# Optimization experiments

Hardware: AMD Instinct MI355X
Metric: run time of the kernel (lower is better)

Reference implementation:

```python
import jax, jax.numpy as jnp
import numpy as np

NUM_EXPERTS = 8
TOP_K = 2

def setup_inputs() -> dict:
    key = jax.random.key(0)
    ks = jax.random.split(key, 5)
    B, S, H, I, E = 4, 2048, 1024, 2816, NUM_EXPERTS
    return {
        "hidden_states": jax.random.normal(ks[0], (B, S, H), dtype=jnp.float32),
        "gate_w": jax.random.normal(ks[1], (H, E), dtype=jnp.float32) / np.sqrt(H),
        "w_gate": jax.random.normal(ks[2], (E, H, I), dtype=jnp.float32) / np.sqrt(H),
        "w_up": jax.random.normal(ks[3], (E, H, I), dtype=jnp.float32) / np.sqrt(H),
        "w_down": jax.random.normal(ks[4], (E, I, H), dtype=jnp.float32) / np.sqrt(I),
    }

def reference(hidden_states, gate_w, w_gate, w_up, w_down):
    B, S, H = hidden_states.shape
    x = hidden_states.reshape(-1, H)                      # [T, H]
    router_logits = x @ gate_w                            # [T, E]
    probs = jax.nn.softmax(router_logits.astype(jnp.float32), axis=-1)
    topk_w, sel = jax.lax.top_k(probs, TOP_K)             # [T, K]
    topk_w = topk_w / jnp.sum(topk_w, axis=-1, keepdims=True)
    topk_w = topk_w.astype(x.dtype)
    out = jnp.zeros_like(x)
    for e in range(NUM_EXPERTS):
        # combine weight for this expert per token (0 if not routed)
        we = jnp.sum(jnp.where(sel == e, topk_w, 0.0), axis=-1)  # [T]
        h = jax.nn.silu(x @ w_gate[e]) * (x @ w_up[e])           # [T, I]
        out = out + (h @ w_down[e]) * we[:, None]
    return out.reshape(B, S, H), router_logits
```

## Files before the change

### kernel.cpp

```cpp
#include <hip/hip_runtime.h>
#include <hip/hip_bf16.h>
#include <stdint.h>

typedef unsigned short u16;
typedef unsigned int u32;

#define T_TOK 8192
#define H_DIM 1024
#define I_DIM 2816
#define NE 8

typedef __bf16 bf16x8 __attribute__((ext_vector_type(8)));
typedef float f32x4 __attribute__((ext_vector_type(4)));

union F8 { uint4 v; bf16x8 f; u32 w[4]; };

__device__ __forceinline__ u16 f2bf(float f) {
    u32 u = __float_as_uint(f);
    u32 r = u + 0x7FFFu + ((u >> 16) & 1u);
    return (u16)(r >> 16);
}
__device__ __forceinline__ u32 pkbf(float a, float b) {
    float2 f; f.x = a; f.y = b;
    __hip_bfloat162 h = __float22bfloat162_rn(f);
    union { __hip_bfloat162 h2; u32 w; } cv; cv.h2 = h;
    return cv.w;
}

__device__ __forceinline__ void g2l16(const void* g, void* l) {
    __builtin_amdgcn_global_load_lds(
        (const __attribute__((address_space(1))) u32*)g,
        (__attribute__((address_space(3))) u32*)l, 16, 0, 0);
}

__global__ void zero_cnt_kernel(int* __restrict__ cnt) {
    if (threadIdx.x < NE) cnt[threadIdx.x] = 0;
}

__global__ void __launch_bounds__(256) zero_out_kernel(float* __restrict__ out0) {
    int gid = blockIdx.x * 256 + threadIdx.x;
    f32x4 z = {0.f, 0.f, 0.f, 0.f};
    ((f32x4*)out0)[gid] = z;
}

__global__ void __launch_bounds__(256) xcvt_kernel(const float* __restrict__ x, u16* __restrict__ xb) {
    size_t gid = (size_t)blockIdx.x * 256 + threadIdx.x;
    const float4* s = (const float4*)x + gid * 2;
    float4 a = s[0], b = s[1];
    uint4 o;
    o.x = pkbf(a.x, a.y); o.y = pkbf(a.z, a.w);
    o.z = pkbf(b.x, b.y); o.w = pkbf(b.z, b.w);
    ((uint4*)xb)[gid] = o;
}

__global__ void __launch_bounds__(256)
pack_kernel(const float* __restrict__ src, u32* __restrict__ dst, int K, int N) {
    int e = blockIdx.z;
    int n0 = blockIdx.x * 64;
    int r0 = blockIdx.y * 128;
    __shared__ float sT[128][65];
    int tid = threadIdx.x;
    const float* sp = src + ((size_t)e * K + r0) * N + n0;
#pragma unroll
    for (int rep = 0; rep < 8; rep++) {
        int row = rep * 16 + (tid >> 4);
        int n4 = (tid & 15) * 4;
        float4 v = *(const float4*)(sp + (size_t)row * N + n4);
        sT[row][n4] = v.x; sT[row][n4 + 1] = v.y; sT[row][n4 + 2] = v.z; sT[row][n4 + 3] = v.w;
    }
    __syncthreads();
    int n = tid >> 2, q = tid & 3;
    u32* dp = dst + ((size_t)e * N + n0 + n) * (size_t)(K >> 1) + (r0 >> 1) + q * 16;
    uint4 o[4];
    u32* ow = (u32*)o;
#pragma unroll
    for (int j = 0; j < 16; j++) {
        int k2 = q * 16 + j;
        ow[j] = pkbf(sT[2 * k2][n], sT[2 * k2 + 1][n]);
    }
#pragma unroll
    for (int j = 0; j < 4; j++) ((uint4*)dp)[j] = o[j];
}

__global__ void __launch_bounds__(256)
router_kernel(const float* __restrict__ x, const float* __restrict__ gw,
              float* __restrict__ logits_out, float* __restrict__ wbuf,
              int* __restrict__ cnt, int* __restrict__ idxlist) {
    int lane = threadIdx.x & 63;
    int t = blockIdx.x * 4 + (threadIdx.x >> 6);
    const float* xr = x + (size_t)t * H_DIM;
    float acc[NE];
#pragma unroll
    for (int e = 0; e < NE; e++) acc[e] = 0.f;
#pragma unroll
    for (int i = 0; i < 16; i++) {
        int hh = i * 64 + lane;
        float xv = xr[hh];
        const float4* grow = (const float4*)(gw + (size_t)hh * NE);
        float4 g0 = grow[0], g1 = grow[1];
        acc[0] += xv * g0.x; acc[1] += xv * g0.y;
        acc[2] += xv * g0.z; acc[3] += xv * g0.w;
        acc[4] += xv * g1.x; acc[5] += xv * g1.y;
        acc[6] += xv * g1.z; acc[7] += xv * g1.w;
    }
#pragma unroll
    for (int m = 32; m >= 1; m >>= 1) {
#pragma unroll
        for (int e = 0; e < NE; e++) acc[e] += __shfl_xor(acc[e], m, 64);
    }
    if (lane == 0) {
        float mx = acc[0];
#pragma unroll
        for (int e = 1; e < NE; e++) mx = fmaxf(mx, acc[e]);
        float p[NE];
#pragma unroll
        for (int e = 0; e < NE; e++) p[e] = __expf(acc[e] - mx);
        float4 l0, l1;
        l0.x = acc[0]; l0.y = acc[1]; l0.z = acc[2]; l0.w = acc[3];
        l1.x = acc[4]; l1.y = acc[5]; l1.z = acc[6]; l1.w = acc[7];
        float4* lrow_p = (float4*)(logits_out + (size_t)t * NE);
        lrow_p[0] = l0; lrow_p[1] = l1;
        int a = 0; float pa = p[0];
#pragma unroll
        for (int e = 1; e < NE; e++) if (p[e] > pa) { a = e; pa = p[e]; }
        int b = -1; float pb = -1.f;
#pragma unroll
        for (int e = 0; e < NE; e++) if (e != a && p[e] > pb) { b = e; pb = p[e]; }
        if (b < 0) { b = a ^ 1; pb = p[b]; }
        float inv = 1.f / (pa + pb);
        wbuf[2 * t]     = pa * inv;
        wbuf[2 * t + 1] = pb * inv;
        int pos = atomicAdd(&cnt[a], 1); idxlist[a * T_TOK + pos] = 2 * t;
        pos = atomicAdd(&cnt[b], 1);     idxlist[b * T_TOK + pos] = 2 * t + 1;
    }
}

__global__ void __launch_bounds__(256, 2)
gateup_kernel(const u16* __restrict__ xb, const u32* __restrict__ wgp,
              const u32* __restrict__ wup, const int* __restrict__ cnt,
              const int* __restrict__ idxlist, u16* __restrict__ hchunk,
              int nbase, int nlen) {
    int NN = nlen >> 7;
    int pid = blockIdx.x;
    int xcd = pid & 7;
    int j = pid >> 3;
    int m = j & 63;
    int gs = j >> 6;
    int g = xcd + (gs << 3);
    int e = g / NN;
    int nb = g - e * NN;
    int c = cnt[e];
    int m0 = m * 128;
    if (m0 >= c) return;
    int n0l = nb * 128;
    int n0g = nbase + n0l;

    __shared__ alignas(16) u16 sA[2][128 * 64];
    __shared__ alignas(16) u32 sB[2][128 * 32];
    int tid = threadIdx.x;
    int wv = tid >> 6;

    int arow = tid >> 3;
    int csw = tid & 7;
    const u16* aP[4];
#pragma unroll
    for (int p = 0; p < 4; p++) {
        int jj = m0 + p * 32 + arow; if (jj > c - 1) jj = c - 1;
        int slot = idxlist[e * T_TOK + jj];
        aP[p] = xb + (size_t)(slot >> 1) * H_DIM + ((csw ^ (arow & 7)) << 3);
    }
    size_t bn = (size_t)e * I_DIM + n0g + arow;
    int bsw = (csw ^ (arow & 7)) << 2;
    const u32* bgB = wgp + bn * 512 + bsw;
    const u32* buB = wup + bn * 512 + bsw;

    auto stage = [&](int k0, int buf, const u32* bB) {
#pragma unroll
        for (int p = 0; p < 4; p++)
            g2l16(aP[p] + k0, &sA[buf][(p * 256 + wv * 64) * 8]);
#pragma unroll
        for (int p = 0; p < 4; p++)
            g2l16(bB + (size_t)p * 32 * 512 + (k0 >> 1), &sB[buf][(p * 256 + wv * 64) * 4]);
    };

    int lane = tid & 63;
    int wm = (tid >> 7) & 1, wn = (tid >> 6) & 1;
    int lrow = lane & 15, quad = lane >> 4;
    f32x4 zero = {0.f, 0.f, 0.f, 0.f};
    f32x4 accg[4][4], accu[4][4];
#pragma unroll
    for (int mi = 0; mi < 4; mi++)
#pragma unroll
        for (int ni = 0; ni < 4; ni++) { accg[mi][ni] = zero; accu[mi][ni] = zero; }

    auto run_pass = [&](const u32* bBc, const u32* bBn, f32x4 (&acc)[4][4]) {
#pragma unroll 2
        for (int k0 = 0; k0 < H_DIM; k0 += 64) {
            int buf = (k0 >> 6) & 1;
            __syncthreads();
            if (k0 + 64 < H_DIM) stage(k0 + 64, buf ^ 1, bBc);
            else if (bBn)        stage(0, buf ^ 1, bBn);
#pragma unroll
            for (int kk = 0; kk < 2; kk++) {
                int cb = kk * 4 + quad;
                bf16x8 af[4]; F8 bf[4];
#pragma unroll
                for (int i = 0; i < 4; i++) {
                    int ra = wm * 64 + i * 16 + lrow;
                    af[i] = *(const bf16x8*)&sA[buf][(size_t)(ra * 8 + (cb ^ (ra & 7))) * 8];
                    int n = wn * 64 + i * 16 + lrow;
                    bf[i].v = *(const uint4*)&sB[buf][(size_t)(n * 8 + (cb ^ (n & 7))) * 4];
                }
#pragma unroll
                for (int mi = 0; mi < 4; mi++)
#pragma unroll
                    for (int ni = 0; ni < 4; ni++)
                        acc[mi][ni] = __builtin_amdgcn_mfma_f32_16x16x32_bf16(af[mi], bf[ni].f, acc[mi][ni], 0, 0, 0);
            }
        }
    };

    stage(0, 0, bgB);
    run_pass(bgB, buB, accg);
    run_pass(buB, nullptr, accu);

    u16* hT = &sA[0][0];
    __syncthreads();
#pragma unroll
    for (int mi = 0; mi < 4; mi++) {
#pragma unroll
        for (int r = 0; r < 4; r++) {
            int row = wm * 64 + mi * 16 + quad * 4 + r;
            int swz = (row & 7) << 3;
#pragma unroll
            for (int ni = 0; ni < 4; ni++) {
                int col = wn * 64 + ni * 16 + lrow;
                float gv = accg[mi][ni][r], uv = accu[mi][ni][r];
                float hv = gv * uv / (1.f + __expf(-gv));
                hT[row * 128 + (col ^ swz)] = f2bf(hv);
            }
        }
    }
    __syncthreads();
    {
        int row = tid & 127, half = tid >> 7;
        int grow = m0 + row;
        if (grow < c) {
            int slot = idxlist[e * T_TOK + grow];
            u16* dst = hchunk + (size_t)slot * nlen + n0l + half * 64;
            int swz = (row & 7) << 3;
#pragma unroll
            for (int j2 = 0; j2 < 8; j2++) {
                int colb = half * 64 + j2 * 8;
                *(uint4*)(dst + j2 * 8) = *(const uint4*)&hT[row * 128 + (colb ^ swz)];
            }
        }
    }
}

__global__ void __launch_bounds__(256, 2)
down_kernel(const u16* __restrict__ hchunk, const u32* __restrict__ wdp,
            const int* __restrict__ cnt, const int* __restrict__ idxlist,
            const float* __restrict__ wbuf, float* __restrict__ out0,
            float* __restrict__ ybuf, int kbase, int klen, int beta) {
    int pid = blockIdx.x;
    int xcd = pid & 7;
    int j = pid >> 3;
    int m = j & 63;
    int gs = j >> 6;
    int g = xcd + (gs << 3);
    int e = g >> 3;
    int nb = g & 7;
    int c = cnt[e];
    int m0 = m * 128;
    if (m0 >= c) return;
    int n0 = nb * 128;

    __shared__ alignas(16) u16 sA[2][128 * 64];
    __shared__ alignas(16) u32 sB[2][128 * 32];
    int tid = threadIdx.x;
    int wv = tid >> 6;

    int arow = tid >> 3;
    int csw = tid & 7;
    const u16* aP[4];
#pragma unroll
    for (int p = 0; p < 4; p++) {
        int jj = m0 + p * 32 + arow; if (jj > c - 1) jj = c - 1;
        int slot = idxlist[e * T_TOK + jj];
        aP[p] = hchunk + (size_t)slot * klen + ((csw ^ (arow & 7)) << 3);
    }
    int bsw = (csw ^ (arow & 7)) << 2;
    const u32* bB = wdp + ((size_t)e * H_DIM + n0 + arow) * 1408 + (kbase >> 1) + bsw;

    auto stage = [&](int k0, int buf) {
#pragma unroll
        for (int p = 0; p < 4; p++)
            g2l16(aP[p] + k0, &sA[buf][(p * 256 + wv * 64) * 8]);
#pragma unroll
        for (int p = 0; p < 4; p++)
            g2l16(bB + (size_t)p * 32 * 1408 + (k0 >> 1), &sB[buf][(p * 256 + wv * 64) * 4]);
    };

    int lane = tid & 63;
    int wm = (tid >> 7) & 1, wn = (tid >> 6) & 1;
    int lrow = lane & 15, quad = lane >> 4;
    f32x4 zero = {0.f, 0.f, 0.f, 0.f};
    f32x4 acc[4][4];
#pragma unroll
    for (int mi = 0; mi < 4; mi++)
#pragma unroll
        for (int ni = 0; ni < 4; ni++) acc[mi][ni] = zero;

    stage(0, 0);
#pragma unroll 2
    for (int k0 = 0; k0 < klen; k0 += 64) {
        int buf = (k0 >> 6) & 1;
        __syncthreads();
        if (k0 + 64 < klen) stage(k0 + 64, buf ^ 1);
#pragma unroll
        for (int kk = 0; kk < 2; kk++) {
            int cb = kk * 4 + quad;
            bf16x8 af[4]; F8 bf[4];
#pragma unroll
            for (int i = 0; i < 4; i++) {
                int ra = wm * 64 + i * 16 + lrow;
                af[i] = *(const bf16x8*)&sA[buf][(size_t)(ra * 8 + (cb ^ (ra & 7))) * 8];
                int n = wn * 64 + i * 16 + lrow;
                bf[i].v = *(const uint4*)&sB[buf][(size_t)(n * 8 + (cb ^ (n & 7))) * 4];
            }
#pragma unroll
            for (int mi = 0; mi < 4; mi++)
#pragma unroll
                for (int ni = 0; ni < 4; ni++)
                    acc[mi][ni] = __builtin_amdgcn_mfma_f32_16x16x32_bf16(af[mi], bf[ni].f, acc[mi][ni], 0, 0, 0);
        }
    }
#pragma unroll
    for (int mi = 0; mi < 4; mi++) {
#pragma unroll
        for (int r = 0; r < 4; r++) {
            int grow = m0 + wm * 64 + mi * 16 + quad * 4 + r;
            if (grow < c) {
                int slot = idxlist[e * T_TOK + grow];
                if (ybuf) {
                    float* yrow = ybuf + (size_t)slot * H_DIM + n0 + wn * 64 + lrow;
                    if (beta) {
#pragma unroll
                        for (int ni = 0; ni < 4; ni++) yrow[ni * 16] += acc[mi][ni][r];
                    } else {
#pragma unroll
                        for (int ni = 0; ni < 4; ni++) yrow[ni * 16] = acc[mi][ni][r];
                    }
                } else {
                    float w = wbuf[slot];
                    float* yrow = out0 + (size_t)(slot >> 1) * H_DIM + n0 + wn * 64 + lrow;
#pragma unroll
                    for (int ni = 0; ni < 4; ni++)
                        atomicAdd(&yrow[ni * 16], w * acc[mi][ni][r]);
                }
            }
        }
    }
}

__global__ void __launch_bounds__(256)
combine_kernel(const float* __restrict__ ybuf, const float* __restrict__ wbuf,
               float* __restrict__ out0) {
    int gid = blockIdx.x * 256 + threadIdx.x;
    int t = gid >> 8;
    int h4 = gid & 255;
    float w0 = wbuf[2 * t], w1 = wbuf[2 * t + 1];
    f32x4 a = ((const f32x4*)(ybuf + (size_t)(2 * t) * H_DIM))[h4];
    f32x4 b = ((const f32x4*)(ybuf + (size_t)(2 * t + 1) * H_DIM))[h4];
    f32x4 o;
#pragma unroll
    for (int i = 0; i < 4; i++) o[i] = w0 * a[i] + w1 * b[i];
    ((f32x4*)(out0 + (size_t)t * H_DIM))[h4] = o;
}

extern "C" void kernel_launch(void* const* d_in, const int* in_sizes, int n_in,
                              void* d_out, int out_size, void* d_ws, size_t ws_size,
                              hipStream_t stream) {
    (void)in_sizes; (void)n_in; (void)out_size;
    const float* x  = (const float*)d_in[0];
    const float* gw = (const float*)d_in[1];
    const float* wg = (const float*)d_in[2];
    const float* wu = (const float*)d_in[3];
    const float* wd = (const float*)d_in[4];
    float* out = (float*)d_out;
    float* logits = out + (size_t)T_TOK * H_DIM;
    char* ws = (char*)d_ws;

    size_t off = 0;
    auto take = [&](size_t sz) { char* p = ws + off; off += (sz + 255) & ~(size_t)255; return p; };
    int* cnt      = (int*)take(NE * 4);
    int* idxlist  = (int*)take((size_t)NE * T_TOK * 4);
    float* wbuf   = (float*)take((size_t)2 * T_TOK * 4);
    u16* xb       = (u16*)take((size_t)T_TOK * H_DIM * 2);
    u32* wgp      = (u32*)take((size_t)NE * I_DIM * 512 * 4);
    u32* wup      = (u32*)take((size_t)NE * I_DIM * 512 * 4);
    u32* wdp      = (u32*)take((size_t)NE * H_DIM * 1408 * 4);
    float* ybuf = nullptr;
    size_t ybytes = (size_t)2 * T_TOK * H_DIM * 4;
    size_t minh   = (size_t)2 * T_TOK * 128 * 2 + 256;
    if (ws_size >= off + ybytes + minh) ybuf = (float*)take(ybytes);
    int ich = I_DIM;
    while (ich > 128 && off + (size_t)2 * T_TOK * ich * 2 > ws_size) ich -= 128;
    u16* hchunk = (u16*)(ws + off);

    zero_cnt_kernel<<<1, 64, 0, stream>>>(cnt);
    if (!ybuf) zero_out_kernel<<<T_TOK * H_DIM / 4 / 256, 256, 0, stream>>>(out);
    pack_kernel<<<dim3(I_DIM / 64, H_DIM / 128, NE), 256, 0, stream>>>(wg, wgp, H_DIM, I_DIM);
    pack_kernel<<<dim3(I_DIM / 64, H_DIM / 128, NE), 256, 0, stream>>>(wu, wup, H_DIM, I_DIM);
    pack_kernel<<<dim3(H_DIM / 64, I_DIM / 128, NE), 256, 0, stream>>>(wd, wdp, I_DIM, H_DIM);
    xcvt_kernel<<<T_TOK * H_DIM / 8 / 256, 256, 0, stream>>>(x, xb);
    router_kernel<<<T_TOK / 4, 256, 0, stream>>>(x, gw, logits, wbuf, cnt, idxlist);
    for (int base = 0; base < I_DIM; base += ich) {
        int len = I_DIM - base; if (len > ich) len = ich;
        int NN = len / 128;
        gateup_kernel<<<64 * NN * NE, 256, 0, stream>>>(xb, wgp, wup, cnt, idxlist, hchunk, base, len);
        down_kernel<<<64 * 8 * NE, 256, 0, stream>>>(hchunk, wdp, cnt, idxlist, wbuf, out, ybuf, base, len, base > 0 ? 1 : 0);
    }
    if (ybuf) combine_kernel<<<T_TOK * H_DIM / 4 / 256, 256, 0, stream>>>(ybuf, wbuf, out);
}
```

Baseline: 1.011 ms.

## Use 256-row tiles with 512 threads and fuse gate/up GEMM passes

Both expert GEMM kernels move from 128x128 tiles on 256 threads to 256x128 tiles on 512 threads (8 waves), and the grid mapping is reduced to match. The gate/up kernel now stages gate and up weight tiles together and accumulates both in one K loop, sharing each A-tile load, instead of running two sequential passes over K. The aim is to cut redundant activation loads and raise data reuse per block. In exchange, shared memory per block roughly doubles, and launch_bounds(512,2) with 128 accumulator registers per thread in gateup may cause register spills or lower occupancy.

```diff
diff --git a/kernel.cpp b/kernel.cpp
--- a/kernel.cpp
+++ b/kernel.cpp
@@ -135,7 +135,7 @@
     }
 }
 
-__global__ void __launch_bounds__(256, 2)
+__global__ void __launch_bounds__(512, 2)
 gateup_kernel(const u16* __restrict__ xb, const u32* __restrict__ wgp,
               const u32* __restrict__ wup, const int* __restrict__ cnt,
               const int* __restrict__ idxlist, u16* __restrict__ hchunk,
@@ -144,19 +144,20 @@
     int pid = blockIdx.x;
     int xcd = pid & 7;
     int j = pid >> 3;
-    int m = j & 63;
-    int gs = j >> 6;
+    int m = j & 31;
+    int gs = j >> 5;
     int g = xcd + (gs << 3);
     int e = g / NN;
     int nb = g - e * NN;
     int c = cnt[e];
-    int m0 = m * 128;
+    int m0 = m * 256;
     if (m0 >= c) return;
     int n0l = nb * 128;
     int n0g = nbase + n0l;
 
-    __shared__ alignas(16) u16 sA[2][128 * 64];
-    __shared__ alignas(16) u32 sB[2][128 * 32];
+    __shared__ alignas(16) u16 sA[2][256 * 64];
+    __shared__ alignas(16) u32 sBg[2][128 * 32];
+    __shared__ alignas(16) u32 sBu[2][128 * 32];
     int tid = threadIdx.x;
     int wv = tid >> 6;
 
@@ -165,7 +166,7 @@
     const u16* aP[4];
 #pragma unroll
     for (int p = 0; p < 4; p++) {
-        int jj = m0 + p * 32 + arow; if (jj > c - 1) jj = c - 1;
+        int jj = m0 + p * 64 + arow; if (jj > c - 1) jj = c - 1;
         int slot = idxlist[e * T_TOK + jj];
         aP[p] = xb + (size_t)(slot >> 1) * H_DIM + ((csw ^ (arow & 7)) << 3);
     }
@@ -174,17 +175,20 @@
     const u32* bgB = wgp + bn * 512 + bsw;
     const u32* buB = wup + bn * 512 + bsw;
 
-    auto stage = [&](int k0, int buf, const u32* bB) {
+    auto stage = [&](int k0, int buf) {
 #pragma unroll
         for (int p = 0; p < 4; p++)
-            g2l16(aP[p] + k0, &sA[buf][(p * 256 + wv * 64) * 8]);
-#pragma unroll
-        for (int p = 0; p < 4; p++)
-            g2l16(bB + (size_t)p * 32 * 512 + (k0 >> 1), &sB[buf][(p * 256 + wv * 64) * 4]);
+            g2l16(aP[p] + k0, &sA[buf][(p * 64 + wv * 8) * 64]);
+#pragma unroll
+        for (int p2 = 0; p2 < 2; p2++)
+            g2l16(bgB + (size_t)p2 * 64 * 512 + (k0 >> 1), &sBg[buf][(p2 * 64 + wv * 8) * 32]);
+#pragma unroll
+        for (int p2 = 0; p2 < 2; p2++)
+            g2l16(buB + (size_t)p2 * 64 * 512 + (k0 >> 1), &sBu[buf][(p2 * 64 + wv * 8) * 32]);
     };
 
     int lane = tid & 63;
-    int wm = (tid >> 7) & 1, wn = (tid >> 6) & 1;
+    int wm = wv >> 1, wn = wv & 1;
     int lrow = lane & 15, quad = lane >> 4;
     f32x4 zero = {0.f, 0.f, 0.f, 0.f};
     f32x4 accg[4][4], accu[4][4];
@@ -193,36 +197,33 @@
 #pragma unroll
         for (int ni = 0; ni < 4; ni++) { accg[mi][ni] = zero; accu[mi][ni] = zero; }
 
-    auto run_pass = [&](const u32* bBc, const u32* bBn, f32x4 (&acc)[4][4]) {
+    stage(0, 0);
 #pragma unroll 2
-        for (int k0 = 0; k0 < H_DIM; k0 += 64) {
-            int buf = (k0 >> 6) & 1;
-            __syncthreads();
-            if (k0 + 64 < H_DIM) stage(k0 + 64, buf ^ 1, bBc);
-            else if (bBn)        stage(0, buf ^ 1, bBn);
-#pragma unroll
-            for (int kk = 0; kk < 2; kk++) {
-                int cb = kk * 4 + quad;
-                bf16x8 af[4]; F8 bf[4];
-#pragma unroll
-                for (int i = 0; i < 4; i++) {
-                    int ra = wm * 64 + i * 16 + lrow;
-                    af[i] = *(const bf16x8*)&sA[buf][(size_t)(ra * 8 + (cb ^ (ra & 7))) * 8];
-                    int n = wn * 64 + i * 16 + lrow;
-                    bf[i].v = *(const uint4*)&sB[buf][(size_t)(n * 8 + (cb ^ (n & 7))) * 4];
+    for (int k0 = 0; k0 < H_DIM; k0 += 64) {
+        int buf = (k0 >> 6) & 1;
+        __syncthreads();
+        if (k0 + 64 < H_DIM) stage(k0 + 64, buf ^ 1);
+#pragma unroll
+        for (int kk = 0; kk < 2; kk++) {
+            int cb = kk * 4 + quad;
+            bf16x8 af[4]; F8 bg[4], bu[4];
+#pragma unroll
+            for (int i = 0; i < 4; i++) {
+                int ra = wm * 64 + i * 16 + lrow;
+                af[i] = *(const bf16x8*)&sA[buf][(size_t)(ra * 8 + (cb ^ (ra & 7))) * 8];
+                int n = wn * 64 + i * 16 + lrow;
+                bg[i].v = *(const uint4*)&sBg[buf][(size_t)(n * 8 + (cb ^ (n & 7))) * 4];
+                bu[i].v = *(const uint4*)&sBu[buf][(size_t)(n * 8 + (cb ^ (n & 7))) * 4];
+            }
+#pragma unroll
+            for (int mi = 0; mi < 4; mi++)
+#pragma unroll
+                for (int ni = 0; ni < 4; ni++) {
+                    accg[mi][ni] = __builtin_amdgcn_mfma_f32_16x16x32_bf16(af[mi], bg[ni].f, accg[mi][ni], 0, 0, 0);
+                    accu[mi][ni] = __builtin_amdgcn_mfma_f32_16x16x32_bf16(af[mi], bu[ni].f, accu[mi][ni], 0, 0, 0);
                 }
-#pragma unroll
-                for (int mi = 0; mi < 4; mi++)
-#pragma unroll
-                    for (int ni = 0; ni < 4; ni++)
-                        acc[mi][ni] = __builtin_amdgcn_mfma_f32_16x16x32_bf16(af[mi], bf[ni].f, acc[mi][ni], 0, 0, 0);
-            }
         }
-    };
-
-    stage(0, 0, bgB);
-    run_pass(bgB, buB, accg);
-    run_pass(buB, nullptr, accu);
+    }
 
     u16* hT = &sA[0][0];
     __syncthreads();
@@ -243,7 +244,7 @@
     }
     __syncthreads();
     {
-        int row = tid & 127, half = tid >> 7;
+        int row = tid >> 1, half = tid & 1;
         int grow = m0 + row;
         if (grow < c) {
             int slot = idxlist[e * T_TOK + grow];
@@ -258,7 +259,7 @@
     }
 }
 
-__global__ void __launch_bounds__(256, 2)
+__global__ void __launch_bounds__(512, 2)
 down_kernel(const u16* __restrict__ hchunk, const u32* __restrict__ wdp,
             const int* __restrict__ cnt, const int* __restrict__ idxlist,
             const float* __restrict__ wbuf, float* __restrict__ out0,
@@ -266,17 +267,17 @@
     int pid = blockIdx.x;
     int xcd = pid & 7;
     int j = pid >> 3;
-    int m = j & 63;
-    int gs = j >> 6;
+    int m = j & 31;
+    int gs = j >> 5;
     int g = xcd + (gs << 3);
     int e = g >> 3;
     int nb = g & 7;
     int c = cnt[e];
-    int m0 = m * 128;
+    int m0 = m * 256;
     if (m0 >= c) return;
     int n0 = nb * 128;
 
-    __shared__ alignas(16) u16 sA[2][128 * 64];
+    __shared__ alignas(16) u16 sA[2][256 * 64];
     __shared__ alignas(16) u32 sB[2][128 * 32];
     int tid = threadIdx.x;
     int wv = tid >> 6;
@@ -286,7 +287,7 @@
     const u16* aP[4];
 #pragma unroll
     for (int p = 0; p < 4; p++) {
-        int jj = m0 + p * 32 + arow; if (jj > c - 1) jj = c - 1;
+        int jj = m0 + p * 64 + arow; if (jj > c - 1) jj = c - 1;
         int slot = idxlist[e * T_TOK + jj];
         aP[p] = hchunk + (size_t)slot * klen + ((csw ^ (arow & 7)) << 3);
     }
@@ -296,14 +297,14 @@
     auto stage = [&](int k0, int buf) {
 #pragma unroll
         for (int p = 0; p < 4; p++)
-            g2l16(aP[p] + k0, &sA[buf][(p * 256 + wv * 64) * 8]);
-#pragma unroll
-        for (int p = 0; p < 4; p++)
-            g2l16(bB + (size_t)p * 32 * 1408 + (k0 >> 1), &sB[buf][(p * 256 + wv * 64) * 4]);
+            g2l16(aP[p] + k0, &sA[buf][(p * 64 + wv * 8) * 64]);
+#pragma unroll
+        for (int p2 = 0; p2 < 2; p2++)
+            g2l16(bB + (size_t)p2 * 64 * 1408 + (k0 >> 1), &sB[buf][(p2 * 64 + wv * 8) * 32]);
     };
 
     int lane = tid & 63;
-    int wm = (tid >> 7) & 1, wn = (tid >> 6) & 1;
+    int wm = wv >> 1, wn = wv & 1;
     int lrow = lane & 15, quad = lane >> 4;
     f32x4 zero = {0.f, 0.f, 0.f, 0.f};
     f32x4 acc[4][4];
@@ -419,8 +420,8 @@
     for (int base = 0; base < I_DIM; base += ich) {
         int len = I_DIM - base; if (len > ich) len = ich;
         int NN = len / 128;
-        gateup_kernel<<<64 * NN * NE, 256, 0, stream>>>(xb, wgp, wup, cnt, idxlist, hchunk, base, len);
-        down_kernel<<<64 * 8 * NE, 256, 0, stream>>>(hchunk, wdp, cnt, idxlist, wbuf, out, ybuf, base, len, base > 0 ? 1 : 0);
+        gateup_kernel<<<8 * 32 * NN, 512, 0, stream>>>(xb, wgp, wup, cnt, idxlist, hchunk, base, len);
+        down_kernel<<<8 * 32 * 8, 512, 0, stream>>>(hchunk, wdp, cnt, idxlist, wbuf, out, ybuf, base, len, base > 0 ? 1 : 0);
     }
     if (ybuf) combine_kernel<<<T_TOK * H_DIM / 4 / 256, 256, 0, stream>>>(ybuf, wbuf, out);
 }
```

New measurement: 1.196 ms. +18.3%, slower.
